# Kernel optimization log

Hardware: AMD Instinct MI355X
Metric: run time of the kernel (lower is better)

## Reference

```python
import jax, jax.numpy as jnp
import numpy as np

N_NODES = 20000
N_EDGES = 100000
STALK_DIM = 32
N_EDGE_ATTR = 32
N_FEAT = 32


def setup_inputs() -> dict:
    key = jax.random.key(0)
    k1, k2, k3, k4 = jax.random.split(key, 4)
    x = jax.random.normal(k1, (N_NODES, STALK_DIM, N_FEAT), dtype=jnp.float32)
    edge_index = jax.random.randint(k2, (2, N_EDGES), 0, N_NODES, dtype=jnp.int64)
    edge_attr = jax.random.normal(k3, (N_EDGES, N_EDGE_ATTR), dtype=jnp.float32)
    # basis restriction maps: (n_edge_attr, 2, d, d), scaled by 1/stalk_dim as in __init__
    restriction_maps = jax.random.normal(k4, (N_EDGE_ATTR, 2, STALK_DIM, STALK_DIM), dtype=jnp.float32) / STALK_DIM
    return {"x": x, "edge_index": edge_index, "edge_attr": edge_attr, "restriction_maps": restriction_maps}


def reference(x, edge_index, edge_attr, restriction_maps):
    n_nodes, d, _ = x.shape
    n_attr = restriction_maps.shape[0]
    # per-edge restriction maps via linear combination of basis maps
    # F: (E, 2, d, d)
    F = (edge_attr @ restriction_maps.reshape(n_attr, 2 * d * d)).reshape(-1, 2, d, d)
    F_left = F[:, 0]   # (E, d, d)
    F_right = F[:, 1]  # (E, d, d)
    # gather node features onto edges
    x_left = x[edge_index[0]]   # (E, d, f)
    x_right = x[edge_index[1]]  # (E, d, f)
    # coboundary: dx = F_left @ x_left - F_right @ x_right
    dx = jnp.einsum('eij,ejf->eif', F_left, x_left) - jnp.einsum('eij,ejf->eif', F_right, x_right)
    # boundary (delta^T dx): transpose-apply and scatter-add to nodes
    x_e_left = jnp.einsum('eji,ejf->eif', F_left, dx)    # F_left^T @ dx
    x_e_right = jnp.einsum('eji,ejf->eif', F_right, dx)  # F_right^T @ dx
    x_out = jax.ops.segment_sum(x_e_left, edge_index[0], num_segments=n_nodes)
    x_out = x_out - jax.ops.segment_sum(x_e_right, edge_index[1], num_segments=n_nodes)
    return x_out
```

## Files before the change

### kernel.cpp

```cpp
#include <hip/hip_runtime.h>
#include <hip/hip_bf16.h>

#define NN 20000
#define NE 100000
#define SLOTS 16
#define FSTRIDE 2056

typedef __attribute__((ext_vector_type(8))) short bf16x8;
typedef __attribute__((ext_vector_type(4))) float f32x4;
typedef __attribute__((ext_vector_type(16))) float f32x16;
typedef __attribute__((ext_vector_type(2))) unsigned uint2v;
typedef __attribute__((ext_vector_type(4))) unsigned uint4v;

#define WS_RBFT 0u
#define WS_FLAG 131072u
#define WS_OFF  131328u
#define WS_CUR  (WS_OFF + 4u*(NN+1))
#define WS_CNT  (WS_CUR + 4u*NN)
#define WS_INC  (WS_CNT + 4u*NN)
#define WS_CSR_END ((size_t)WS_INC + 8u*NE)
#define WS_XT   ((WS_CSR_END + 4095u) & ~(size_t)4095u)
#define WS_XT_END (WS_XT + (size_t)NN * 2048u * 2u)

__device__ __forceinline__ unsigned short f2bf(float f) {
    unsigned u = __float_as_uint(f);
    u += 0x7fffu + ((u >> 16) & 1u);
    return (unsigned short)(u >> 16);
}

__device__ __forceinline__ unsigned pack2bf(float a, float b) {
    union { __hip_bfloat162 h; unsigned u; } q;
    q.h = __float22bfloat162_rn(make_float2(a, b));
    return q.u;
}

__device__ __forceinline__ bf16x8 bneg8(bf16x8 v) {
    union { bf16x8 s; uint4v u; } a; a.s = v;
    a.u[0] ^= 0x80008000u; a.u[1] ^= 0x80008000u;
    a.u[2] ^= 0x80008000u; a.u[3] ^= 0x80008000u;
    return a.s;
}

__global__ void prep_rbf_kernel(const float* __restrict__ R, unsigned short* __restrict__ RbfT,
                                int* __restrict__ flag) {
    int idx = blockIdx.x * blockDim.x + threadIdx.x;
    if (idx == 0) *flag = 0;
    if (idx >= 2048 * 32) return;
    int pos = idx >> 5;
    int a = idx & 31;
    RbfT[idx] = f2bf(R[a * 2048 + pos]);
}

__global__ void detect_kernel(const unsigned* __restrict__ w, int* __restrict__ flag) {
    int k = blockIdx.x * blockDim.x + threadIdx.x;
    if (k < NE && w[2 * k + 1] != 0) atomicOr(flag, 1);
}

__device__ __forceinline__ void decode_edge(const void* eidx, int use64, int e, int& src, int& dst) {
    if (use64) {
        const long long* p = (const long long*)eidx;
        src = (int)p[e]; dst = (int)p[NE + e];
    } else {
        const int* p = (const int*)eidx;
        src = p[e]; dst = p[NE + e];
    }
}

__global__ void count_kernel(const void* __restrict__ eidx, const int* __restrict__ flag,
                             unsigned* __restrict__ cnt) {
    int e = blockIdx.x * blockDim.x + threadIdx.x;
    if (e >= NE) return;
    int src, dst;
    decode_edge(eidx, *flag == 0, e, src, dst);
    if ((unsigned)src < NN) atomicAdd(&cnt[src], 1u);
    if ((unsigned)dst < NN) atomicAdd(&cnt[dst], 1u);
}

__global__ __launch_bounds__(1024) void scan_kernel(const unsigned* __restrict__ cnt,
                                                    unsigned* __restrict__ off,
                                                    unsigned* __restrict__ cur) {
    __shared__ unsigned sd[1024];
    const int t = threadIdx.x;
    unsigned vals[20];
    unsigned s = 0;
#pragma unroll
    for (int j = 0; j < 20; ++j) {
        int idx = t * 20 + j;
        unsigned v = (idx < NN) ? cnt[idx] : 0u;
        vals[j] = s; s += v;
    }
    sd[t] = s;
    __syncthreads();
    for (int d = 1; d < 1024; d <<= 1) {
        unsigned v = (t >= d) ? sd[t - d] : 0u;
        __syncthreads();
        sd[t] += v;
        __syncthreads();
    }
    unsigned base = (t > 0) ? sd[t - 1] : 0u;
#pragma unroll
    for (int j = 0; j < 20; ++j) {
        int idx = t * 20 + j;
        if (idx < NN) { unsigned o = base + vals[j]; off[idx] = o; cur[idx] = o; }
    }
    if (t == 1023) off[NN] = sd[1023];
}

__global__ void scatter_kernel(const void* __restrict__ eidx, const int* __restrict__ flag,
                               unsigned* __restrict__ cur, unsigned* __restrict__ inc) {
    int e = blockIdx.x * blockDim.x + threadIdx.x;
    if (e >= NE) return;
    int src, dst;
    decode_edge(eidx, *flag == 0, e, src, dst);
    if ((unsigned)src < NN) { unsigned p = atomicAdd(&cur[src], 1u); inc[p] = (unsigned)e; }
    if ((unsigned)dst < NN) { unsigned p = atomicAdd(&cur[dst], 1u); inc[p] = (unsigned)e | 0x80000000u; }
}

__global__ __launch_bounds__(256) void xpose_kernel(const float* __restrict__ x,
                                                    unsigned short* __restrict__ xT) {
    __shared__ float tile[4][32][33];
    const int t = threadIdx.x, sub = t >> 6, lane = t & 63;
    const int n = blockIdx.x * 4 + sub;
    const int row = lane >> 1, half = (lane & 1) * 16;
    const float* xp = x + (size_t)n * 1024 + row * 32 + half;
    float* tp = &tile[sub][row][half];
#pragma unroll
    for (int c = 0; c < 4; ++c)
        *(f32x4*)(tp + 4 * c) = *(const f32x4*)(xp + 4 * c);
    __syncthreads();
    const int f = lane >> 1, k0 = (lane & 1) * 16;
    unsigned w[8];
#pragma unroll
    for (int m = 0; m < 8; ++m) {
        unsigned lo = (unsigned)f2bf(tile[sub][k0 + 2 * m][f]);
        unsigned hi = (unsigned)f2bf(tile[sub][k0 + 2 * m + 1][f]);
        w[m] = lo | (hi << 16);
    }
    unsigned short* op = xT + (size_t)n * 2048 + f * 32 + k0;
    uint4v v0 = {w[0], w[1], w[2], w[3]};
    uint4v v1 = {w[4], w[5], w[6], w[7]};
    *(uint4v*)op = v0;
    *(uint4v*)(op + 8) = v1;
}

template<bool XT>
__global__ __launch_bounds__(256, 2) void sheaf_node(
    const float* __restrict__ x,
    const unsigned short* __restrict__ xTbuf,
    const void* __restrict__ eidx_raw,
    const float* __restrict__ ea,
    const unsigned short* __restrict__ RbfT,
    const int* __restrict__ flag,
    const unsigned* __restrict__ off,
    const unsigned* __restrict__ inc,
    float* __restrict__ out)
{
    __shared__ __align__(16) unsigned short F_lds[SLOTS * FSTRIDE];
    __shared__ __align__(16) unsigned dx_lds32[4 * 512];
    __shared__ int slot_src[SLOTS], slot_dst[SLOTS], slot_side[SLOTS], slot_e[SLOTS];

    const int n    = blockIdx.x;
    const int tid  = threadIdx.x;
    const int lane = tid & 63;
    const int wv   = tid >> 6;
    const int use64 = (*flag == 0);

    const unsigned start = off[n];
    const int deg = (int)(off[n + 1] - start);

    const int r31 = lane & 31;
    const int hi  = lane >> 5;
    const int kb  = hi * 8;
    unsigned* dx2 = dx_lds32 + wv * 512;

    f32x16 acc;
#pragma unroll
    for (int r = 0; r < 16; ++r) acc[r] = 0.f;

    for (int base = 0; base < deg; base += SLOTS) {
        __syncthreads();
        if (tid < SLOTS) {
            int p = base + tid;
            if (p < deg) {
                unsigned v = inc[start + p];
                int e = (int)(v & 0x7fffffffu);
                int s, d; decode_edge(eidx_raw, use64, e, s, d);
                if ((unsigned)s >= NN) s = 0;
                if ((unsigned)d >= NN) d = 0;
                slot_e[tid] = e; slot_src[tid] = s; slot_dst[tid] = d;
                slot_side[tid] = (int)(v >> 31);
            } else slot_e[tid] = -1;
        }
        __syncthreads();

        bf16x8 pre0[4], pre1[4], pre2[4], pre3[4];
        if constexpr (XT) {
#pragma unroll
            for (int s = 0; s < 4; ++s) {
                const int si = wv + 4 * s;
                if (base + si < deg) {
                    const unsigned short* xls = xTbuf + (size_t)slot_src[si] * 2048 + r31 * 32 + kb;
                    const unsigned short* xrs = xTbuf + (size_t)slot_dst[si] * 2048 + r31 * 32 + kb;
                    pre0[s] = *(const bf16x8*)xls;
                    pre1[s] = *(const bf16x8*)(xls + 16);
                    pre2[s] = *(const bf16x8*)xrs;
                    pre3[s] = *(const bf16x8*)(xrs + 16);
                }
            }
        }

        {
            const int slot = lane & 15;
            const int ab   = (lane >> 4) * 8;
            const int e    = slot_e[slot];
            bf16x8 bfrag = {0, 0, 0, 0, 0, 0, 0, 0};
            if (e >= 0) {
                const float* eap = ea + (size_t)e * 32 + ab;
                f32x4 a0 = *(const f32x4*)eap;
                f32x4 a1 = *(const f32x4*)(eap + 4);
#pragma unroll
                for (int j = 0; j < 4; ++j) { bfrag[j] = (short)f2bf(a0[j]); bfrag[4 + j] = (short)f2bf(a1[j]); }
            }
            unsigned short* fdst = F_lds + slot * FSTRIDE;
            const int pg = (lane >> 4) * 4;
#pragma unroll 8
            for (int t = 0; t < 32; ++t) {
                const int pos_base = wv * 512 + t * 16;
                bf16x8 afrag = *(const bf16x8*)(RbfT + (size_t)(pos_base + (lane & 15)) * 32 + ab);
                f32x4 c = {0.f, 0.f, 0.f, 0.f};
                c = __builtin_amdgcn_mfma_f32_16x16x32_bf16(afrag, bfrag, c, 0, 0, 0);
                const int posb = pos_base + pg;
                const int side = posb >> 10;
                const int ijb  = posb & 1023;
                const int i    = ijb >> 5;
                const int soff = ijb ^ ((i & 7) << 3);
                uint2v wp = {pack2bf(c[0], c[1]), pack2bf(c[2], c[3])};
                *(uint2v*)(fdst + side * 1024 + soff) = wp;
            }
        }
        __syncthreads();

#pragma unroll
        for (int s = 0; s < 4; ++s) {
            const int si = wv + 4 * s;
            if (base + si >= deg) break;
            const int src  = slot_src[si];
            const int dst  = slot_dst[si];
            const int side = slot_side[si];

            bf16x8 xlf0, xlf1, xrf0, xrf1;
            if constexpr (XT) {
                xlf0 = pre0[s];
                xlf1 = pre1[s];
                xrf0 = bneg8(pre2[s]);
                xrf1 = bneg8(pre3[s]);
            } else {
                const float* xl = x + (size_t)src * 1024 + r31;
                const float* xr = x + (size_t)dst * 1024 + r31;
#pragma unroll
                for (int j = 0; j < 8; ++j) {
                    xlf0[j] = (short)f2bf(xl[(kb + j) * 32]);
                    xlf1[j] = (short)f2bf(xl[(16 + kb + j) * 32]);
                    xrf0[j] = (short)f2bf(-xr[(kb + j) * 32]);
                    xrf1[j] = (short)f2bf(-xr[(16 + kb + j) * 32]);
                }
            }

            const unsigned short* Fl = F_lds + si * FSTRIDE;
            const unsigned short* Fr = Fl + 1024;
            const int rbase = r31 * 32;
            const int rsw   = (r31 & 7) << 3;
            bf16x8 fl0 = *(const bf16x8*)(Fl + ((rbase + kb) ^ rsw));
            bf16x8 fl1 = *(const bf16x8*)(Fl + ((rbase + 16 + kb) ^ rsw));
            bf16x8 fr0 = *(const bf16x8*)(Fr + ((rbase + kb) ^ rsw));
            bf16x8 fr1 = *(const bf16x8*)(Fr + ((rbase + 16 + kb) ^ rsw));

            f32x16 dacc;
#pragma unroll
            for (int r = 0; r < 16; ++r) dacc[r] = 0.f;
            dacc = __builtin_amdgcn_mfma_f32_32x32x16_bf16(fl0, xlf0, dacc, 0, 0, 0);
            dacc = __builtin_amdgcn_mfma_f32_32x32x16_bf16(fl1, xlf1, dacc, 0, 0, 0);
            dacc = __builtin_amdgcn_mfma_f32_32x32x16_bf16(fr0, xrf0, dacc, 0, 0, 0);
            dacc = __builtin_amdgcn_mfma_f32_32x32x16_bf16(fr1, xrf1, dacc, 0, 0, 0);

            const unsigned smask = side ? 0x80008000u : 0u;
#pragma unroll
            for (int m = 0; m < 8; ++m) {
                const int wi = (m & 1) + 4 * (m >> 1) + 2 * hi;
                dx2[wi * 32 + r31] = pack2bf(dacc[2 * m], dacc[2 * m + 1]) ^ smask;
            }
            unsigned wa[4], wb[4];
#pragma unroll
            for (int m = 0; m < 4; ++m) {
                wa[m] = dx2[(4 * hi + m) * 32 + r31];
                wb[m] = dx2[(8 + 4 * hi + m) * 32 + r31];
            }
            union { uint4v u; bf16x8 s; } pa, pb;
            pa.u = (uint4v){wa[0], wa[1], wa[2], wa[3]};
            pb.u = (uint4v){wb[0], wb[1], wb[2], wb[3]};
            const bf16x8 dxf0 = pa.s, dxf1 = pb.s;

            const unsigned short* Fs = side ? Fr : Fl;
            bf16x8 fT0, fT1;
#pragma unroll
            for (int j = 0; j < 8; ++j) {
                const int k0 = kb + j, k1 = 16 + kb + j;
                fT0[j] = (short)Fs[(k0 * 32 + r31) ^ ((k0 & 7) << 3)];
                fT1[j] = (short)Fs[(k1 * 32 + r31) ^ ((k1 & 7) << 3)];
            }
            acc = __builtin_amdgcn_mfma_f32_32x32x16_bf16(fT0, dxf0, acc, 0, 0, 0);
            acc = __builtin_amdgcn_mfma_f32_32x32x16_bf16(fT1, dxf1, acc, 0, 0, 0);
        }
    }

    __syncthreads();
    float* red = (float*)F_lds;
#pragma unroll
    for (int r = 0; r < 16; ++r) {
        const int row = (r & 3) + 8 * (r >> 2) + 4 * hi;
        red[wv * 1024 + row * 32 + r31] = acc[r];
    }
    __syncthreads();
    {
        const int p4 = tid * 4;
        f32x4 s0 = *(const f32x4*)(red + p4);
        f32x4 s1 = *(const f32x4*)(red + 1024 + p4);
        f32x4 s2 = *(const f32x4*)(red + 2048 + p4);
        f32x4 s3 = *(const f32x4*)(red + 3072 + p4);
        f32x4 o;
#pragma unroll
        for (int j = 0; j < 4; ++j) o[j] = (s0[j] + s1[j]) + (s2[j] + s3[j]);
        *(f32x4*)(out + (size_t)n * 1024 + p4) = o;
    }
}

__global__ __launch_bounds__(512, 4) void sheaf_atomic(
    const float* __restrict__ x,
    const void* __restrict__ eidx_raw,
    const float* __restrict__ ea,
    const unsigned short* __restrict__ RbfT,
    const int* __restrict__ flag,
    float* __restrict__ out)
{
    __shared__ __align__(16) unsigned short F_lds[16 * 2048];
    __shared__ __align__(16) unsigned short dx_lds[8 * 1024];

    const int tid  = threadIdx.x;
    const int lane = tid & 63;
    const int wv   = tid >> 6;
    const int e0   = blockIdx.x * 16;
    const int use64 = (*flag == 0);

    {
        const int arow = lane & 15;
        const int ab   = (lane >> 4) * 8;
        const float* eap = ea + (size_t)(e0 + arow) * 32 + ab;
        f32x4 a0 = *(const f32x4*)eap;
        f32x4 a1 = *(const f32x4*)(eap + 4);
        bf16x8 afrag;
#pragma unroll
        for (int j = 0; j < 4; ++j) { afrag[j] = (short)f2bf(a0[j]); afrag[4 + j] = (short)f2bf(a1[j]); }
        const int pcol  = lane & 15;
        const int ebase = (lane >> 4) * 4;
#pragma unroll
        for (int t = 0; t < 16; ++t) {
            const int pos = wv * 256 + t * 16 + pcol;
            bf16x8 bfrag = *(const bf16x8*)(RbfT + pos * 32 + ab);
            f32x4 c = {0.f, 0.f, 0.f, 0.f};
            c = __builtin_amdgcn_mfma_f32_16x16x32_bf16(afrag, bfrag, c, 0, 0, 0);
            const int side = pos >> 10;
            const int ij   = pos & 1023;
            const int i    = ij >> 5;
            const int soff = side * 1024 + (ij ^ ((i & 7) << 3));
#pragma unroll
            for (int r = 0; r < 4; ++r)
                F_lds[(ebase + r) * 2048 + soff] = f2bf(c[r]);
        }
    }
    __syncthreads();

    const int r31 = lane & 31;
    const int hi  = lane >> 5;
    const int kb  = hi * 8;
    unsigned short* dxb = dx_lds + wv * 1024;

#pragma unroll 1
    for (int sub = 0; sub < 2; ++sub) {
        const int el = wv * 2 + sub;
        const int e  = e0 + el;
        int src, dst;
        decode_edge(eidx_raw, use64, e, src, dst);
        if ((unsigned)src >= NN || (unsigned)dst >= NN) continue;

        const float* xl = x + (size_t)src * 1024 + r31;
        const float* xr = x + (size_t)dst * 1024 + r31;
        bf16x8 xlf0, xlf1, xrf0, xrf1;
#pragma unroll
        for (int j = 0; j < 8; ++j) {
            xlf0[j] = (short)f2bf(xl[(kb + j) * 32]);
            xlf1[j] = (short)f2bf(xl[(16 + kb + j) * 32]);
            xrf0[j] = (short)f2bf(-xr[(kb + j) * 32]);
            xrf1[j] = (short)f2bf(-xr[(16 + kb + j) * 32]);
        }
        const unsigned short* Fl = F_lds + el * 2048;
        const unsigned short* Fr = Fl + 1024;
        const int rbase = r31 * 32;
        const int rsw   = (r31 & 7) << 3;
        bf16x8 fl0 = *(const bf16x8*)(Fl + ((rbase + kb) ^ rsw));
        bf16x8 fl1 = *(const bf16x8*)(Fl + ((rbase + 16 + kb) ^ rsw));
        bf16x8 fr0 = *(const bf16x8*)(Fr + ((rbase + kb) ^ rsw));
        bf16x8 fr1 = *(const bf16x8*)(Fr + ((rbase + 16 + kb) ^ rsw));

        f32x16 dacc;
#pragma unroll
        for (int r = 0; r < 16; ++r) dacc[r] = 0.f;
        dacc = __builtin_amdgcn_mfma_f32_32x32x16_bf16(fl0, xlf0, dacc, 0, 0, 0);
        dacc = __builtin_amdgcn_mfma_f32_32x32x16_bf16(fl1, xlf1, dacc, 0, 0, 0);
        dacc = __builtin_amdgcn_mfma_f32_32x32x16_bf16(fr0, xrf0, dacc, 0, 0, 0);
        dacc = __builtin_amdgcn_mfma_f32_32x32x16_bf16(fr1, xrf1, dacc, 0, 0, 0);

#pragma unroll
        for (int r = 0; r < 16; ++r) {
            const int row = (r & 3) + 8 * (r >> 2) + 4 * hi;
            dxb[row * 32 + r31] = f2bf(dacc[r]);
        }
        bf16x8 dxf0, dxf1;
#pragma unroll
        for (int j = 0; j < 8; ++j) {
            dxf0[j] = (short)dxb[(kb + j) * 32 + r31];
            dxf1[j] = (short)dxb[(16 + kb + j) * 32 + r31];
        }

        bf16x8 flT0, flT1;
#pragma unroll
        for (int j = 0; j < 8; ++j) {
            const int k0 = kb + j, k1 = 16 + kb + j;
            flT0[j] = (short)Fl[(k0 * 32 + r31) ^ ((k0 & 7) << 3)];
            flT1[j] = (short)Fl[(k1 * 32 + r31) ^ ((k1 & 7) << 3)];
        }
        f32x16 yl;
#pragma unroll
        for (int r = 0; r < 16; ++r) yl[r] = 0.f;
        yl = __builtin_amdgcn_mfma_f32_32x32x16_bf16(flT0, dxf0, yl, 0, 0, 0);
        yl = __builtin_amdgcn_mfma_f32_32x32x16_bf16(flT1, dxf1, yl, 0, 0, 0);
        float* outs = out + (size_t)src * 1024 + r31;
#pragma unroll
        for (int r = 0; r < 16; ++r) {
            const int row = (r & 3) + 8 * (r >> 2) + 4 * hi;
            atomicAdd(outs + row * 32, yl[r]);
        }

        bf16x8 frT0, frT1;
#pragma unroll
        for (int j = 0; j < 8; ++j) {
            const int k0 = kb + j, k1 = 16 + kb + j;
            frT0[j] = (short)Fr[(k0 * 32 + r31) ^ ((k0 & 7) << 3)];
            frT1[j] = (short)Fr[(k1 * 32 + r31) ^ ((k1 & 7) << 3)];
        }
        f32x16 yr;
#pragma unroll
        for (int r = 0; r < 16; ++r) yr[r] = 0.f;
        yr = __builtin_amdgcn_mfma_f32_32x32x16_bf16(frT0, dxf0, yr, 0, 0, 0);
        yr = __builtin_amdgcn_mfma_f32_32x32x16_bf16(frT1, dxf1, yr, 0, 0, 0);
        float* outd = out + (size_t)dst * 1024 + r31;
#pragma unroll
        for (int r = 0; r < 16; ++r) {
            const int row = (r & 3) + 8 * (r >> 2) + 4 * hi;
            atomicAdd(outd + row * 32, -yr[r]);
        }
    }
}

extern "C" void kernel_launch(void* const* d_in, const int* in_sizes, int n_in,
                              void* d_out, int out_size, void* d_ws, size_t ws_size,
                              hipStream_t stream) {
    const float* x  = (const float*)d_in[0];
    const void* eidx = d_in[1];
    const float* ea = (const float*)d_in[2];
    const float* R  = (const float*)d_in[3];
    float* out = (float*)d_out;
    char* ws = (char*)d_ws;

    unsigned short* RbfT = (unsigned short*)(ws + WS_RBFT);
    int* flag = (int*)(ws + WS_FLAG);

    prep_rbf_kernel<<<256, 256, 0, stream>>>(R, RbfT, flag);
    detect_kernel<<<(NE + 255) / 256, 256, 0, stream>>>((const unsigned*)eidx, flag);

    if (ws_size >= WS_CSR_END) {
        unsigned* off = (unsigned*)(ws + WS_OFF);
        unsigned* cur = (unsigned*)(ws + WS_CUR);
        unsigned* cnt = (unsigned*)(ws + WS_CNT);
        unsigned* inc = (unsigned*)(ws + WS_INC);

        hipMemsetAsync(cnt, 0, 4u * NN, stream);
        count_kernel<<<(NE + 255) / 256, 256, 0, stream>>>(eidx, flag, cnt);
        scan_kernel<<<1, 1024, 0, stream>>>(cnt, off, cur);
        scatter_kernel<<<(NE + 255) / 256, 256, 0, stream>>>(eidx, flag, cur, inc);

        if (ws_size >= WS_XT_END) {
            unsigned short* xT = (unsigned short*)(ws + WS_XT);
            xpose_kernel<<<NN / 4, 256, 0, stream>>>(x, xT);
            sheaf_node<true><<<NN, 256, 0, stream>>>(x, xT, eidx, ea, RbfT, flag, off, inc, out);
        } else {
            sheaf_node<false><<<NN, 256, 0, stream>>>(x, nullptr, eidx, ea, RbfT, flag, off, inc, out);
        }
    } else {
        hipMemsetAsync(d_out, 0, (size_t)out_size * sizeof(float), stream);
        sheaf_atomic<<<NE / 16, 512, 0, stream>>>(x, eidx, ea, RbfT, flag, out);
    }
}
```

Measured before the change: 399.0 us.

## Split incidence list into fixed 16-entry blocks with partial-sum combine pass

Replaces the one-block-per-node kernel with a kernel that processes fixed chunks of 16 CSR incidences, which balances load regardless of node degree and keeps all 16 F slots busy. Segments fully contained in a block write directly to the output. Boundary segments write bf16 partial sums to a workspace buffer, and a new combine kernel adds them per node and zero-fills empty nodes. This adds an extra nodeOf array, a partial buffer, an extra launch, and bf16 rounding on the partial sums.

```diff
diff --git a/kernel.cpp b/kernel.cpp
--- a/kernel.cpp
+++ b/kernel.cpp
@@ -3,6 +3,8 @@
 
 #define NN 20000
 #define NE 100000
+#define NINC (2 * NE)
+#define NB (NINC / 16)
 #define SLOTS 16
 #define FSTRIDE 2056
 
@@ -18,9 +20,12 @@
 #define WS_CUR  (WS_OFF + 4u*(NN+1))
 #define WS_CNT  (WS_CUR + 4u*NN)
 #define WS_INC  (WS_CNT + 4u*NN)
-#define WS_CSR_END ((size_t)WS_INC + 8u*NE)
+#define WS_NODE (WS_INC + 4u*NINC)
+#define WS_CSR_END ((size_t)WS_NODE + 4u*NINC)
 #define WS_XT   ((WS_CSR_END + 4095u) & ~(size_t)4095u)
 #define WS_XT_END (WS_XT + (size_t)NN * 2048u * 2u)
+#define WS_PB   ((WS_XT_END + 4095u) & ~(size_t)4095u)
+#define WS_PB_END (WS_PB + (size_t)NB * 2u * 2048u)
 
 __device__ __forceinline__ unsigned short f2bf(float f) {
     unsigned u = __float_as_uint(f);
@@ -32,6 +37,10 @@
     union { __hip_bfloat162 h; unsigned u; } q;
     q.h = __float22bfloat162_rn(make_float2(a, b));
     return q.u;
+}
+
+__device__ __forceinline__ float bf2f(unsigned s) {
+    return __uint_as_float(s << 16);
 }
 
 __device__ __forceinline__ bf16x8 bneg8(bf16x8 v) {
@@ -107,13 +116,14 @@
 }
 
 __global__ void scatter_kernel(const void* __restrict__ eidx, const int* __restrict__ flag,
-                               unsigned* __restrict__ cur, unsigned* __restrict__ inc) {
+                               unsigned* __restrict__ cur, unsigned* __restrict__ inc,
+                               unsigned* __restrict__ nodeOf) {
     int e = blockIdx.x * blockDim.x + threadIdx.x;
     if (e >= NE) return;
     int src, dst;
     decode_edge(eidx, *flag == 0, e, src, dst);
-    if ((unsigned)src < NN) { unsigned p = atomicAdd(&cur[src], 1u); inc[p] = (unsigned)e; }
-    if ((unsigned)dst < NN) { unsigned p = atomicAdd(&cur[dst], 1u); inc[p] = (unsigned)e | 0x80000000u; }
+    if ((unsigned)src < NN) { unsigned p = atomicAdd(&cur[src], 1u); inc[p] = (unsigned)e; nodeOf[p] = (unsigned)src; }
+    if ((unsigned)dst < NN) { unsigned p = atomicAdd(&cur[dst], 1u); inc[p] = (unsigned)e | 0x80000000u; nodeOf[p] = (unsigned)dst; }
 }
 
 __global__ __launch_bounds__(256) void xpose_kernel(const float* __restrict__ x,
@@ -141,6 +151,209 @@
     uint4v v1 = {w[4], w[5], w[6], w[7]};
     *(uint4v*)op = v0;
     *(uint4v*)(op + 8) = v1;
+}
+
+__global__ __launch_bounds__(256, 2) void sheaf_inc(
+    const unsigned short* __restrict__ xTbuf,
+    const void* __restrict__ eidx_raw,
+    const float* __restrict__ ea,
+    const unsigned short* __restrict__ RbfT,
+    const int* __restrict__ flag,
+    const unsigned* __restrict__ off,
+    const unsigned* __restrict__ inc,
+    const unsigned* __restrict__ nodeOf,
+    float* __restrict__ out,
+    unsigned short* __restrict__ pbuf)
+{
+    __shared__ __align__(16) unsigned short F_lds[SLOTS * FSTRIDE];
+    __shared__ __align__(16) unsigned dx_lds32[4 * 512];
+    __shared__ int slot_src[SLOTS], slot_dst[SLOTS], slot_side[SLOTS], slot_e[SLOTS], slot_n[SLOTS];
+
+    const int b    = blockIdx.x;
+    const int p0   = b * 16;
+    const int tid  = threadIdx.x;
+    const int lane = tid & 63;
+    const int wv   = tid >> 6;
+    const int use64 = (*flag == 0);
+
+    const int r31 = lane & 31;
+    const int hi  = lane >> 5;
+    const int kb  = hi * 8;
+    unsigned* dx2 = dx_lds32 + wv * 512;
+
+    if (tid < SLOTS) {
+        unsigned v = inc[p0 + tid];
+        int e = (int)(v & 0x7fffffffu);
+        int s, d; decode_edge(eidx_raw, use64, e, s, d);
+        if ((unsigned)s >= NN) s = 0;
+        if ((unsigned)d >= NN) d = 0;
+        slot_e[tid] = e; slot_src[tid] = s; slot_dst[tid] = d;
+        slot_side[tid] = (int)(v >> 31);
+        slot_n[tid] = (int)nodeOf[p0 + tid];
+    }
+    __syncthreads();
+
+    bf16x8 pre0[4], pre1[4], pre2[4], pre3[4];
+#pragma unroll
+    for (int s = 0; s < 4; ++s) {
+        const int si = wv + 4 * s;
+        const unsigned short* xls = xTbuf + (size_t)slot_src[si] * 2048 + r31 * 32 + kb;
+        const unsigned short* xrs = xTbuf + (size_t)slot_dst[si] * 2048 + r31 * 32 + kb;
+        pre0[s] = *(const bf16x8*)xls;
+        pre1[s] = *(const bf16x8*)(xls + 16);
+        pre2[s] = *(const bf16x8*)xrs;
+        pre3[s] = *(const bf16x8*)(xrs + 16);
+    }
+
+    {
+        const int slot = lane & 15;
+        const int ab   = (lane >> 4) * 8;
+        const int e    = slot_e[slot];
+        bf16x8 bfrag;
+        {
+            const float* eap = ea + (size_t)e * 32 + ab;
+            f32x4 a0 = *(const f32x4*)eap;
+            f32x4 a1 = *(const f32x4*)(eap + 4);
+#pragma unroll
+            for (int j = 0; j < 4; ++j) { bfrag[j] = (short)f2bf(a0[j]); bfrag[4 + j] = (short)f2bf(a1[j]); }
+        }
+        unsigned short* fdst = F_lds + slot * FSTRIDE;
+        const int pg = (lane >> 4) * 4;
+#pragma unroll 8
+        for (int t = 0; t < 32; ++t) {
+            const int pos_base = wv * 512 + t * 16;
+            bf16x8 afrag = *(const bf16x8*)(RbfT + (size_t)(pos_base + (lane & 15)) * 32 + ab);
+            f32x4 c = {0.f, 0.f, 0.f, 0.f};
+            c = __builtin_amdgcn_mfma_f32_16x16x32_bf16(afrag, bfrag, c, 0, 0, 0);
+            const int posb = pos_base + pg;
+            const int side = posb >> 10;
+            const int ijb  = posb & 1023;
+            const int i    = ijb >> 5;
+            const int soff = ijb ^ ((i & 7) << 3);
+            uint2v wp = {pack2bf(c[0], c[1]), pack2bf(c[2], c[3])};
+            *(uint2v*)(fdst + side * 1024 + soff) = wp;
+        }
+    }
+    __syncthreads();
+
+#pragma unroll
+    for (int s = 0; s < 4; ++s) {
+        const int si = wv + 4 * s;
+        const int side = slot_side[si];
+
+        bf16x8 xlf0 = pre0[s];
+        bf16x8 xlf1 = pre1[s];
+        bf16x8 xrf0 = bneg8(pre2[s]);
+        bf16x8 xrf1 = bneg8(pre3[s]);
+
+        const unsigned short* Fl = F_lds + si * FSTRIDE;
+        const unsigned short* Fr = Fl + 1024;
+        const int rbase = r31 * 32;
+        const int rsw   = (r31 & 7) << 3;
+        bf16x8 fl0 = *(const bf16x8*)(Fl + ((rbase + kb) ^ rsw));
+        bf16x8 fl1 = *(const bf16x8*)(Fl + ((rbase + 16 + kb) ^ rsw));
+        bf16x8 fr0 = *(const bf16x8*)(Fr + ((rbase + kb) ^ rsw));
+        bf16x8 fr1 = *(const bf16x8*)(Fr + ((rbase + 16 + kb) ^ rsw));
+
+        f32x16 dacc;
+#pragma unroll
+        for (int r = 0; r < 16; ++r) dacc[r] = 0.f;
+        dacc = __builtin_amdgcn_mfma_f32_32x32x16_bf16(fl0, xlf0, dacc, 0, 0, 0);
+        dacc = __builtin_amdgcn_mfma_f32_32x32x16_bf16(fl1, xlf1, dacc, 0, 0, 0);
+        dacc = __builtin_amdgcn_mfma_f32_32x32x16_bf16(fr0, xrf0, dacc, 0, 0, 0);
+        dacc = __builtin_amdgcn_mfma_f32_32x32x16_bf16(fr1, xrf1, dacc, 0, 0, 0);
+
+        const unsigned smask = side ? 0x80008000u : 0u;
+#pragma unroll
+        for (int m = 0; m < 8; ++m) {
+            const int wi = (m & 1) + 4 * (m >> 1) + 2 * hi;
+            dx2[wi * 32 + r31] = pack2bf(dacc[2 * m], dacc[2 * m + 1]) ^ smask;
+        }
+        unsigned wa[4], wb[4];
+#pragma unroll
+        for (int m = 0; m < 4; ++m) {
+            wa[m] = dx2[(4 * hi + m) * 32 + r31];
+            wb[m] = dx2[(8 + 4 * hi + m) * 32 + r31];
+        }
+        union { uint4v u; bf16x8 s; } pa, pb;
+        pa.u = (uint4v){wa[0], wa[1], wa[2], wa[3]};
+        pb.u = (uint4v){wb[0], wb[1], wb[2], wb[3]};
+        const bf16x8 dxf0 = pa.s, dxf1 = pb.s;
+
+        const unsigned short* Fs = side ? Fr : Fl;
+        bf16x8 fT0, fT1;
+#pragma unroll
+        for (int j = 0; j < 8; ++j) {
+            const int k0 = kb + j, k1 = 16 + kb + j;
+            fT0[j] = (short)Fs[(k0 * 32 + r31) ^ ((k0 & 7) << 3)];
+            fT1[j] = (short)Fs[(k1 * 32 + r31) ^ ((k1 & 7) << 3)];
+        }
+        f32x16 y;
+#pragma unroll
+        for (int r = 0; r < 16; ++r) y[r] = 0.f;
+        y = __builtin_amdgcn_mfma_f32_32x32x16_bf16(fT0, dxf0, y, 0, 0, 0);
+        y = __builtin_amdgcn_mfma_f32_32x32x16_bf16(fT1, dxf1, y, 0, 0, 0);
+
+        float* ybuf = (float*)(F_lds + si * FSTRIDE);
+#pragma unroll
+        for (int r = 0; r < 16; ++r) {
+            const int row = (r & 3) + 8 * (r >> 2) + 4 * hi;
+            ybuf[row * 32 + r31] = y[r];
+        }
+    }
+    __syncthreads();
+
+    {
+        const int e4 = tid * 4;
+        int segA = 0;
+        while (segA < SLOTS) {
+            const int n = slot_n[segA];
+            int segB = segA + 1;
+            while (segB < SLOTS && slot_n[segB] == n) ++segB;
+            f32x4 sum = {0.f, 0.f, 0.f, 0.f};
+            for (int s2 = segA; s2 < segB; ++s2) {
+                const f32x4 v = *(const f32x4*)((const float*)(F_lds + s2 * FSTRIDE) + e4);
+#pragma unroll
+                for (int j = 0; j < 4; ++j) sum[j] += v[j];
+            }
+            const unsigned on = off[n], on1 = off[n + 1];
+            const bool complete = ((unsigned)(p0 + segA) == on) && ((unsigned)(p0 + segB) == on1);
+            if (complete) {
+                *(f32x4*)(out + (size_t)n * 1024 + e4) = sum;
+            } else {
+                const int idx = (segA == 0) ? 0 : 1;
+                unsigned short* pb = pbuf + ((size_t)b * 2 + idx) * 1024;
+                uint2v wp = {pack2bf(sum[0], sum[1]), pack2bf(sum[2], sum[3])};
+                *(uint2v*)(pb + e4) = wp;
+            }
+            segA = segB;
+        }
+    }
+}
+
+__global__ __launch_bounds__(256) void combine_kernel(
+    const unsigned* __restrict__ off, const unsigned* __restrict__ nodeOf,
+    const unsigned short* __restrict__ pbuf, float* __restrict__ out)
+{
+    const int n = blockIdx.x;
+    const int e4 = threadIdx.x * 4;
+    const unsigned a = off[n], b = off[n + 1];
+    if (a == b) {
+        f32x4 z = {0.f, 0.f, 0.f, 0.f};
+        *(f32x4*)(out + (size_t)n * 1024 + e4) = z;
+        return;
+    }
+    const unsigned b0 = a >> 4, b1 = (b - 1) >> 4;
+    if (b0 == b1) return;
+    f32x4 sum = {0.f, 0.f, 0.f, 0.f};
+    for (unsigned blk = b0; blk <= b1; ++blk) {
+        const int idx = (nodeOf[blk * 16] == (unsigned)n) ? 0 : 1;
+        const unsigned short* pb = pbuf + ((size_t)blk * 2 + idx) * 1024;
+        uint2v w = *(const uint2v*)(pb + e4);
+        sum[0] += bf2f(w[0] & 0xffffu); sum[1] += bf2f(w[0] >> 16);
+        sum[2] += bf2f(w[1] & 0xffffu); sum[3] += bf2f(w[1] >> 16);
+    }
+    *(f32x4*)(out + (size_t)n * 1024 + e4) = sum;
 }
 
 template<bool XT>
@@ -492,13 +705,20 @@
         unsigned* cur = (unsigned*)(ws + WS_CUR);
         unsigned* cnt = (unsigned*)(ws + WS_CNT);
         unsigned* inc = (unsigned*)(ws + WS_INC);
+        unsigned* nodeOf = (unsigned*)(ws + WS_NODE);
 
         hipMemsetAsync(cnt, 0, 4u * NN, stream);
         count_kernel<<<(NE + 255) / 256, 256, 0, stream>>>(eidx, flag, cnt);
         scan_kernel<<<1, 1024, 0, stream>>>(cnt, off, cur);
-        scatter_kernel<<<(NE + 255) / 256, 256, 0, stream>>>(eidx, flag, cur, inc);
-
-        if (ws_size >= WS_XT_END) {
+        scatter_kernel<<<(NE + 255) / 256, 256, 0, stream>>>(eidx, flag, cur, inc, nodeOf);
+
+        if (ws_size >= WS_PB_END) {
+            unsigned short* xT = (unsigned short*)(ws + WS_XT);
+            unsigned short* pbuf = (unsigned short*)(ws + WS_PB);
+            xpose_kernel<<<NN / 4, 256, 0, stream>>>(x, xT);
+            sheaf_inc<<<NB, 256, 0, stream>>>(xT, eidx, ea, RbfT, flag, off, inc, nodeOf, out, pbuf);
+            combine_kernel<<<NN, 256, 0, stream>>>(off, nodeOf, pbuf, out);
+        } else if (ws_size >= WS_XT_END) {
             unsigned short* xT = (unsigned short*)(ws + WS_XT);
             xpose_kernel<<<NN / 4, 256, 0, stream>>>(x, xT);
             sheaf_node<true><<<NN, 256, 0, stream>>>(x, xT, eidx, ea, RbfT, flag, off, inc, out);
```

Result: faster. 380.8 us (-4.5%).
